# Optimization experiments

Measured on AMD Instinct MI355X. Metric: run time of the kernel, lower is better.

## Reference

```python
import jax, jax.numpy as jnp
import numpy as np

ARRAY_NUM = 1024
LENS_NUM = 16384
LENS_W = 128      # sqrt(LENS_NUM)
SUB = LENS_W // 2  # 64
N_ANG = 121       # fixed by get_weights(): arange(-60, 61)
SLG = 0.1         # side_lobe_gain
VAR_GAIN = 200.0  # 2D lens


def setup_inputs() -> dict:
    key = jax.random.key(0)
    ks = jax.random.split(key, 8)
    u = lambda k, s: jax.random.uniform(k, s, dtype=jnp.float32)
    n = lambda k, s: jax.random.normal(k, s, dtype=jnp.float32)
    return {
        "w_re": u(ks[0], (61, ARRAY_NUM)),
        "w_im": u(ks[1], (61, ARRAY_NUM)),
        "theta_re": u(ks[2], (SUB * SUB, 1)),
        "theta_im": u(ks[3], (SUB * SUB, 1)),
        "G_re": n(ks[4], (ARRAY_NUM, LENS_NUM)),
        "G_im": n(ks[5], (ARRAY_NUM, LENS_NUM)),
        "sv_re": n(ks[6], (LENS_NUM, N_ANG)),
        "sv_im": n(ks[7], (LENS_NUM, N_ANG)),
    }


def _side_lobe_loss(w_re, w_im, theta_re, theta_im, G_re, G_im, sv_re, sv_im):
    w = w_re + 1j * w_im  # [61, A] complex64
    # get_w: clamp |w| to >= 1, normalize, mirror (flipud+fliplr) to full 121 rows
    wn = w / jnp.maximum(jnp.abs(w), 1.0)
    w_full = jnp.concatenate([wn, wn[::-1, ::-1][1:]], axis=0)  # [121, A]

    # get_theta (2D): normalize, tile 4-fold symmetric [128,128], flatten
    theta = theta_re + 1j * theta_im  # [SUB*SUB, 1]
    theta = theta / jnp.abs(theta)
    ts = theta.reshape(SUB, SUB)
    row = jnp.concatenate([ts, ts[:, ::-1]], axis=1)      # [SUB, 2*SUB]
    full = jnp.concatenate([row, row[::-1, :]], axis=0)   # [2*SUB, 2*SUB]
    theta_vec = full.reshape(-1)                          # [LENS_NUM]

    G = G_re + 1j * G_im        # [A, L]
    sv = sv_re + 1j * sv_im     # [L, N_ANG]

    lens_in = w_full @ G                     # [121, L]
    # matmul with diag(theta) == elementwise scale along L (same math)
    sout_c = (lens_in * theta_vec[None, :]) @ sv  # [121, 121]
    sout = (jnp.abs(sout_c) ** 2) / ARRAY_NUM / LENS_NUM

    x = jnp.arange(-60, 61, dtype=jnp.float32)
    weights = (-0.2 / 3600.0) * x ** 2 + 1.0  # [121]

    d = jnp.diagonal(sout)
    diag_out = jnp.sum(d)
    var_loss = VAR_GAIN * jnp.std(d / weights, ddof=1)  # torch.std is unbiased

    # sidelobe cancel: sum of diagonals ti in [-5, 5]
    idx = jnp.arange(N_ANG)
    band = (jnp.abs(idx[:, None] - idx[None, :]) <= 5).astype(sout.dtype)
    diag_sum = jnp.sum(sout * band)
    amp_loss = -diag_out + SLG * (jnp.sum(sout) - diag_sum)

    reg = 0.0 * jnp.mean(jnp.abs(w) ** 2)  # zero-weight reg term, kept for fidelity
    return amp_loss + var_loss + reg


def reference(w_re, w_im, theta_re, theta_im, G_re, G_im, sv_re, sv_im):
    return _side_lobe_loss(w_re, w_im, theta_re, theta_im, G_re, G_im, sv_re, sv_im)
```

## Files before the change

kernel.cpp:

```cpp
#include <hip/hip_runtime.h>
#include <math.h>

#define A_NUM 1024
#define L_NUM 16384
#define NANG  121
#define NPAD  256
#define KSPLIT 32
#define TA 64
#define CHUNK_L 32
#define CHUNK_K 64
#define ROWP 72
#define NCHUNK_G 512

#define WS_TV   0u
#define WS_WF   131072u
#define WS_BT   1122304u
#define WS_PART 19996672u
#define WS_C    53551104u
#define WS_SOUT 54599680u

typedef float  f32x4  __attribute__((ext_vector_type(4)));
typedef short  s16x8  __attribute__((ext_vector_type(8)));
typedef unsigned short u16x8 __attribute__((ext_vector_type(8)));
typedef unsigned short u16x4 __attribute__((ext_vector_type(4)));

__device__ __forceinline__ unsigned short f2bf(float x) {
    union { float f; unsigned u; } v; v.f = x;
    unsigned r = v.u + 0x7fffu + ((v.u >> 16) & 1u);
    return (unsigned short)(r >> 16);
}

#define GLOAD_LDS16(SRC, DST) \
    __builtin_amdgcn_global_load_lds((const __attribute__((address_space(1))) void*)(SRC), \
                                     (__attribute__((address_space(3))) void*)(DST), 16, 0, 0)

__global__ __launch_bounds__(256) void k_prep(
    const float* __restrict__ w_re, const float* __restrict__ w_im,
    const float* __restrict__ th_re, const float* __restrict__ th_im,
    char* __restrict__ wsb)
{
    int idx = blockIdx.x * 256 + threadIdx.x;
    float* tv = (float*)(wsb + WS_TV);
    float* wf = (float*)(wsb + WS_WF);
    if (idx < 16384) {
        int i = idx >> 7, j = idx & 127;
        int r = (i < 64) ? i : 127 - i;
        int c = (j < 64) ? j : 127 - j;
        float tr = th_re[r * 64 + c], ti = th_im[r * 64 + c];
        float inv = rsqrtf(tr * tr + ti * ti);
        tv[2 * idx]     = tr * inv;
        tv[2 * idx + 1] = ti * inv;
    } else if (idx < 16384 + 121 * 1024) {
        int e = idx - 16384;
        int r = e >> 10, a = e & 1023;
        int sr = (r < 61) ? r : 120 - r;
        int sa = (r < 61) ? a : 1023 - a;
        float wr = w_re[sr * 1024 + sa], wi = w_im[sr * 1024 + sa];
        float mag = sqrtf(wr * wr + wi * wi);
        float s = (mag > 1.0f) ? (1.0f / mag) : 1.0f;
        wf[2 * e]     = wr * s;
        wf[2 * e + 1] = wi * s;
    }
}

__global__ __launch_bounds__(256) void k_prep_bt(
    const float* __restrict__ sv_re, const float* __restrict__ sv_im,
    char* __restrict__ wsb)
{
    __shared__ float lsr[32][121];
    __shared__ float lsi[32][121];
    const int cg = blockIdx.x;
    const int t  = threadIdx.x;
    const int lbase = cg * 32;
    for (int e = t; e < 32 * 121; e += 256) {
        int l = e / 121, n = e - l * 121;
        lsr[l][n] = sv_re[(size_t)(lbase + l) * 121 + n];
        lsi[l][n] = sv_im[(size_t)(lbase + l) * 121 + n];
    }
    __syncthreads();
    unsigned short* bt = (unsigned short*)(wsb + WS_BT) + (size_t)cg * (NPAD * ROWP);
    #pragma unroll
    for (int i = 0; i < 18; ++i) {
        int o = t + i * 256;
        int n = o / 18;
        int j = o - n * 18;
        int kl0 = j * 4;
        u16x4 val;
        #pragma unroll
        for (int q = 0; q < 4; ++q) {
            int kl = kl0 + q;
            float v = 0.0f;
            if (kl < 64) {
                int lloc = kl >> 1;
                if (n < 121)                     v = (kl & 1) ? -lsi[lloc][n] : lsr[lloc][n];
                else if (n >= 128 && n < 249)    { int m = n - 128; v = (kl & 1) ? lsr[lloc][m] : lsi[lloc][m]; }
            }
            val[q] = f2bf(v);
        }
        *(u16x4*)&bt[(size_t)o * 4] = val;
    }
}

__global__ __launch_bounds__(256, 2) void k_gemm1(
    const float* __restrict__ G_re, const float* __restrict__ G_im,
    char* __restrict__ wsb)
{
    __shared__ __align__(16) unsigned short lA[TA * ROWP];
    __shared__ __align__(16) unsigned short lB[NPAD * ROWP];

    const int t = threadIdx.x;
    const int bid = blockIdx.x;
    const int kidx  = bid & 31;
    const int atile = bid >> 5;
    const int a0 = atile * TA;
    const int l_begin = kidx * 512;

    const float* __restrict__ tvF = (const float*)(wsb + WS_TV);
    const unsigned short* __restrict__ BtG = (const unsigned short*)(wsb + WS_BT);

    const int wid = t >> 6, lane = t & 63;
    const int arow = lane & 15;
    const int koff = (lane >> 4) * 8;

    const int arow_s = t >> 3;
    const int slot   = t & 7;
    const int lloc   = slot * 4;

    f32x4 acc[4][4];
    #pragma unroll
    for (int j = 0; j < 4; ++j)
        #pragma unroll
        for (int s = 0; s < 4; ++s) acc[j][s] = (f32x4)(0.0f);

    for (int c = 0; c < 16; ++c) {
        const int l0 = l_begin + c * CHUNK_L;
        #pragma unroll
        for (int p = 0; p < 2; ++p) {
            const int a = p * 32 + arow_s;
            const float* grp = G_re + (size_t)(a0 + a) * L_NUM + l0 + lloc;
            const float* gip = G_im + (size_t)(a0 + a) * L_NUM + l0 + lloc;
            float4 gr = *(const float4*)grp;
            float4 gi = *(const float4*)gip;
            const float* tvp = tvF + 2 * (l0 + lloc);
            float4 t0 = *(const float4*)tvp;
            float4 t1 = *(const float4*)(tvp + 4);
            u16x8 pk;
            pk[0] = f2bf(gr.x * t0.x - gi.x * t0.y); pk[1] = f2bf(gr.x * t0.y + gi.x * t0.x);
            pk[2] = f2bf(gr.y * t0.z - gi.y * t0.w); pk[3] = f2bf(gr.y * t0.w + gi.y * t0.z);
            pk[4] = f2bf(gr.z * t1.x - gi.z * t1.y); pk[5] = f2bf(gr.z * t1.y + gi.z * t1.x);
            pk[6] = f2bf(gr.w * t1.z - gi.w * t1.w); pk[7] = f2bf(gr.w * t1.w + gi.w * t1.z);
            *(u16x8*)&lA[a * ROWP + slot * 8] = pk;
        }
        {
            const int cgk = kidx * 16 + c;
            const unsigned short* bsrc = BtG + (size_t)cgk * (NPAD * ROWP);
            unsigned short* ldsb = lB + (size_t)(t & ~63) * 8;
            const unsigned short* gsrc = bsrc + (size_t)t * 8;
            #pragma unroll
            for (int i = 0; i < 9; ++i) {
                GLOAD_LDS16(gsrc + (size_t)i * 2048, ldsb + (size_t)i * 2048);
            }
        }
        __syncthreads();
        #pragma unroll
        for (int kh = 0; kh < 2; ++kh) {
            s16x8 af[4], bf[4];
            #pragma unroll
            for (int j = 0; j < 4; ++j)
                af[j] = *(const s16x8*)&lA[(j * 16 + arow) * ROWP + kh * 32 + koff];
            #pragma unroll
            for (int s = 0; s < 4; ++s)
                bf[s] = *(const s16x8*)&lB[(wid * 64 + s * 16 + arow) * ROWP + kh * 32 + koff];
            #pragma unroll
            for (int j = 0; j < 4; ++j)
                #pragma unroll
                for (int s = 0; s < 4; ++s)
                    acc[j][s] = __builtin_amdgcn_mfma_f32_16x16x32_bf16(af[j], bf[s], acc[j][s], 0, 0, 0);
        }
        __syncthreads();
    }

    float* part = (float*)(wsb + WS_PART) + (size_t)kidx * (A_NUM * NPAD);
    #pragma unroll
    for (int j = 0; j < 4; ++j) {
        #pragma unroll
        for (int s = 0; s < 4; ++s) {
            const int col  = wid * 64 + s * 16 + (lane & 15);
            const int rowb = a0 + j * 16 + (lane >> 4) * 4;
            f32x4 v = acc[j][s];
            #pragma unroll
            for (int r = 0; r < 4; ++r)
                part[(size_t)(rowb + r) * NPAD + col] = v[r];
        }
    }
}

__global__ __launch_bounds__(256) void k_reduce_part(char* __restrict__ wsb)
{
    const int e = blockIdx.x * 256 + threadIdx.x;
    const float* part = (const float*)(wsb + WS_PART);
    float s = 0.0f;
    #pragma unroll
    for (int p = 0; p < KSPLIT; ++p) s += part[(size_t)p * (A_NUM * NPAD) + e];
    ((float*)(wsb + WS_C))[e] = s;
}

__global__ __launch_bounds__(128) void k_gemm2(char* __restrict__ wsb)
{
    __shared__ float lw[2048];
    const int r = blockIdx.x;
    const int t = threadIdx.x;
    const float* wf = (const float*)(wsb + WS_WF) + r * 2048;
    #pragma unroll
    for (int k = 0; k < 16; ++k) lw[t + k * 128] = wf[t + k * 128];
    __syncthreads();
    if (t < 121) {
        const float* __restrict__ C = (const float*)(wsb + WS_C);
        float re = 0.0f, im = 0.0f;
        for (int a = 0; a < 1024; a += 8) {
            #pragma unroll
            for (int u = 0; u < 8; ++u) {
                float wr = lw[2 * (a + u)], wi = lw[2 * (a + u) + 1];
                float br = C[(size_t)(a + u) * NPAD + t];
                float bi = C[(size_t)(a + u) * NPAD + 128 + t];
                re += wr * br - wi * bi;
                im += wr * bi + wi * br;
            }
        }
        ((float*)(wsb + WS_SOUT))[r * 121 + t] = (re * re + im * im) * (1.0f / 16777216.0f);
    }
}

__global__ __launch_bounds__(256) void k_final(const char* __restrict__ wsb, float* __restrict__ out)
{
    __shared__ float red[256];
    __shared__ float red2[256];
    __shared__ float dsh[121];
    const int t = threadIdx.x;
    const float* __restrict__ sout = (const float*)(wsb + WS_SOUT);
    float tot = 0.0f, band = 0.0f;
    for (int e = t; e < NANG * NANG; e += 256) {
        float v = sout[e];
        int i = e / NANG;
        int j = e - i * NANG;
        tot += v;
        int dd = i - j; if (dd < 0) dd = -dd;
        if (dd <= 5) band += v;
        if (dd == 0) dsh[i] = v;
    }
    red[t] = tot; red2[t] = band;
    __syncthreads();
    for (int s2 = 128; s2 > 0; s2 >>= 1) {
        if (t < s2) { red[t] += red[t + s2]; red2[t] += red2[t + s2]; }
        __syncthreads();
    }
    float total = red[0], bandsum = red2[0];
    __syncthreads();

    float d = 0.0f, y = 0.0f;
    if (t < NANG) {
        d = dsh[t];
        float x = (float)(t - 60);
        float wgt = fmaf(x * x, -0.2f / 3600.0f, 1.0f);
        y = d / wgt;
    }
    red[t] = d; red2[t] = y;
    __syncthreads();
    for (int s2 = 128; s2 > 0; s2 >>= 1) {
        if (t < s2) { red[t] += red[t + s2]; red2[t] += red2[t + s2]; }
        __syncthreads();
    }
    float diag_sum = red[0];
    float mean = red2[0] * (1.0f / 121.0f);
    __syncthreads();

    float dev = (t < NANG) ? (y - mean) : 0.0f;
    red[t] = dev * dev;
    __syncthreads();
    for (int s2 = 128; s2 > 0; s2 >>= 1) {
        if (t < s2) { red[t] += red[t + s2]; }
        __syncthreads();
    }
    if (t == 0) {
        float var = red[0] * (1.0f / 120.0f);
        float std_ = sqrtf(var);
        float amp = -diag_sum + 0.1f * (total - bandsum);
        out[0] = amp + 200.0f * std_;
    }
}

extern "C" void kernel_launch(void* const* d_in, const int* in_sizes, int n_in,
                              void* d_out, int out_size, void* d_ws, size_t ws_size,
                              hipStream_t stream)
{
    const float* w_re  = (const float*)d_in[0];
    const float* w_im  = (const float*)d_in[1];
    const float* th_re = (const float*)d_in[2];
    const float* th_im = (const float*)d_in[3];
    const float* G_re  = (const float*)d_in[4];
    const float* G_im  = (const float*)d_in[5];
    const float* sv_re = (const float*)d_in[6];
    const float* sv_im = (const float*)d_in[7];
    char* wsb  = (char*)d_ws;
    float* out = (float*)d_out;

    k_prep<<<dim3(548), 256, 0, stream>>>(w_re, w_im, th_re, th_im, wsb);
    k_prep_bt<<<dim3(NCHUNK_G), 256, 0, stream>>>(sv_re, sv_im, wsb);
    k_gemm1<<<dim3(512), 256, 0, stream>>>(G_re, G_im, wsb);
    k_reduce_part<<<dim3(1024), 256, 0, stream>>>(wsb);
    k_gemm2<<<dim3(121), 128, 0, stream>>>(wsb);
    k_final<<<dim3(1), 256, 0, stream>>>(wsb, out);
}
```

Measured before the change: 265.4 us.

## Double-buffer GEMM1 with larger A tile and parallelize reduce and GEMM2

The main GEMM kernel now uses 512-thread blocks covering 128 A rows and double-buffers both the A and B tiles in LDS. Global loads for the next chunk are issued before the MFMAs on the current chunk, and theta is staged once in LDS. The split-K reduction is vectorized to float4, and GEMM2 splits the 1024-term sum across four thread groups combined through LDS. k_prep_bt is also reworked to write rows directly. The intended gain is less load latency exposure and fewer kernel-level inefficiencies, at the cost of more LDS use and only 256 blocks for GEMM1, which lowers grid-level parallelism.

```diff
diff --git a/kernel.cpp b/kernel.cpp
--- a/kernel.cpp
+++ b/kernel.cpp
@@ -6,11 +6,9 @@
 #define NANG  121
 #define NPAD  256
 #define KSPLIT 32
-#define TA 64
-#define CHUNK_L 32
-#define CHUNK_K 64
+#define TA 128
+#define NCH 16
 #define ROWP 72
-#define NCHUNK_G 512
 
 #define WS_TV   0u
 #define WS_WF   131072u
@@ -19,10 +17,10 @@
 #define WS_C    53551104u
 #define WS_SOUT 54599680u
 
+typedef unsigned short ushort_t;
 typedef float  f32x4  __attribute__((ext_vector_type(4)));
 typedef short  s16x8  __attribute__((ext_vector_type(8)));
 typedef unsigned short u16x8 __attribute__((ext_vector_type(8)));
-typedef unsigned short u16x4 __attribute__((ext_vector_type(4)));
 
 __device__ __forceinline__ unsigned short f2bf(float x) {
     union { float f; unsigned u; } v; v.f = x;
@@ -67,64 +65,127 @@
     const float* __restrict__ sv_re, const float* __restrict__ sv_im,
     char* __restrict__ wsb)
 {
-    __shared__ float lsr[32][121];
-    __shared__ float lsi[32][121];
+    __shared__ float lsr[32][128];
+    __shared__ float lsi[32][128];
     const int cg = blockIdx.x;
     const int t  = threadIdx.x;
     const int lbase = cg * 32;
-    for (int e = t; e < 32 * 121; e += 256) {
-        int l = e / 121, n = e - l * 121;
-        lsr[l][n] = sv_re[(size_t)(lbase + l) * 121 + n];
-        lsi[l][n] = sv_im[(size_t)(lbase + l) * 121 + n];
-    }
-    __syncthreads();
-    unsigned short* bt = (unsigned short*)(wsb + WS_BT) + (size_t)cg * (NPAD * ROWP);
-    #pragma unroll
-    for (int i = 0; i < 18; ++i) {
-        int o = t + i * 256;
-        int n = o / 18;
-        int j = o - n * 18;
-        int kl0 = j * 4;
-        u16x4 val;
-        #pragma unroll
-        for (int q = 0; q < 4; ++q) {
-            int kl = kl0 + q;
-            float v = 0.0f;
-            if (kl < 64) {
-                int lloc = kl >> 1;
-                if (n < 121)                     v = (kl & 1) ? -lsi[lloc][n] : lsr[lloc][n];
-                else if (n >= 128 && n < 249)    { int m = n - 128; v = (kl & 1) ? lsr[lloc][m] : lsi[lloc][m]; }
+    for (int e = t; e < 4096; e += 256) {
+        int l = e >> 7, n = e & 127;
+        float vr = 0.0f, vi = 0.0f;
+        if (n < 121) {
+            vr = sv_re[(size_t)(lbase + l) * 121 + n];
+            vi = sv_im[(size_t)(lbase + l) * 121 + n];
+        }
+        lsr[l][n] = vr; lsi[l][n] = vi;
+    }
+    __syncthreads();
+    ushort_t* bt = (ushort_t*)(wsb + WS_BT) + (size_t)cg * (NPAD * ROWP);
+    const int m = t - 128;
+    #pragma unroll
+    for (int kk = 0; kk < 9; ++kk) {
+        u16x8 v;
+        #pragma unroll
+        for (int qq = 0; qq < 8; ++qq) {
+            int k = kk * 8 + qq;
+            float x = 0.0f;
+            if (k < 64) {
+                int l = k >> 1;
+                if (t < 121)                       x = (k & 1) ? -lsi[l][t] : lsr[l][t];
+                else if (t >= 128 && t < 249)      x = (k & 1) ?  lsr[l][m] : lsi[l][m];
             }
-            val[q] = f2bf(v);
-        }
-        *(u16x4*)&bt[(size_t)o * 4] = val;
-    }
-}
-
-__global__ __launch_bounds__(256, 2) void k_gemm1(
+            v[qq] = f2bf(x);
+        }
+        *(u16x8*)&bt[(size_t)t * ROWP + kk * 8] = v;
+    }
+}
+
+struct APf { float4 gr0, gr1, gi0, gi1; };
+
+__device__ __forceinline__ APf a_issue(const float* __restrict__ G_re, const float* __restrict__ G_im,
+                                       size_t rowbase, int loff) {
+    APf p;
+    const float* grp = G_re + rowbase + loff;
+    const float* gip = G_im + rowbase + loff;
+    p.gr0 = *(const float4*)grp;       p.gr1 = *(const float4*)(grp + 4);
+    p.gi0 = *(const float4*)gip;       p.gi1 = *(const float4*)(gip + 4);
+    return p;
+}
+
+__device__ __forceinline__ void a_store(const APf& p, const float* __restrict__ ltv,
+                                        ushort_t* __restrict__ lAb, int c, int arow, int aslot) {
+    const float* tp = ltv + c * 64 + aslot * 16;
+    float4 t0 = *(const float4*)tp;
+    float4 t1 = *(const float4*)(tp + 4);
+    float4 t2 = *(const float4*)(tp + 8);
+    float4 t3 = *(const float4*)(tp + 12);
+    u16x8 k0, k1;
+    k0[0] = f2bf(p.gr0.x * t0.x - p.gi0.x * t0.y);  k0[1] = f2bf(p.gr0.x * t0.y + p.gi0.x * t0.x);
+    k0[2] = f2bf(p.gr0.y * t0.z - p.gi0.y * t0.w);  k0[3] = f2bf(p.gr0.y * t0.w + p.gi0.y * t0.z);
+    k0[4] = f2bf(p.gr0.z * t1.x - p.gi0.z * t1.y);  k0[5] = f2bf(p.gr0.z * t1.y + p.gi0.z * t1.x);
+    k0[6] = f2bf(p.gr0.w * t1.z - p.gi0.w * t1.w);  k0[7] = f2bf(p.gr0.w * t1.w + p.gi0.w * t1.z);
+    k1[0] = f2bf(p.gr1.x * t2.x - p.gi1.x * t2.y);  k1[1] = f2bf(p.gr1.x * t2.y + p.gi1.x * t2.x);
+    k1[2] = f2bf(p.gr1.y * t2.z - p.gi1.y * t2.w);  k1[3] = f2bf(p.gr1.y * t2.w + p.gi1.y * t2.z);
+    k1[4] = f2bf(p.gr1.z * t3.x - p.gi1.z * t3.y);  k1[5] = f2bf(p.gr1.z * t3.y + p.gi1.z * t3.x);
+    k1[6] = f2bf(p.gr1.w * t3.z - p.gi1.w * t3.w);  k1[7] = f2bf(p.gr1.w * t3.w + p.gi1.w * t3.z);
+    *(u16x8*)&lAb[arow * ROWP + aslot * 16]     = k0;
+    *(u16x8*)&lAb[arow * ROWP + aslot * 16 + 8] = k1;
+}
+
+__device__ __forceinline__ void b_issue(const ushort_t* __restrict__ bsrc,
+                                        ushort_t* __restrict__ lBb, int w, int lane) {
+    #pragma unroll
+    for (int i = 0; i < 5; ++i) {
+        int seg = w + 8 * i;
+        if (seg < 36)
+            GLOAD_LDS16(bsrc + seg * 512 + lane * 8, lBb + seg * 512);
+    }
+}
+
+__device__ __forceinline__ void do_mfma(const ushort_t* __restrict__ lAb, const ushort_t* __restrict__ lBb,
+                                        f32x4 (&acc)[4][4], int wa, int wn, int lane) {
+    const int fr = lane & 15;
+    const int fk = (lane >> 4) * 8;
+    #pragma unroll
+    for (int kh = 0; kh < 2; ++kh) {
+        s16x8 af[4], bf[4];
+        #pragma unroll
+        for (int j = 0; j < 4; ++j)
+            af[j] = *(const s16x8*)&lAb[(wa * 64 + j * 16 + fr) * ROWP + kh * 32 + fk];
+        #pragma unroll
+        for (int s = 0; s < 4; ++s)
+            bf[s] = *(const s16x8*)&lBb[(wn * 64 + s * 16 + fr) * ROWP + kh * 32 + fk];
+        #pragma unroll
+        for (int j = 0; j < 4; ++j)
+            #pragma unroll
+            for (int s = 0; s < 4; ++s)
+                acc[j][s] = __builtin_amdgcn_mfma_f32_16x16x32_bf16(af[j], bf[s], acc[j][s], 0, 0, 0);
+    }
+}
+
+__global__ __launch_bounds__(512, 2) void k_gemm1(
     const float* __restrict__ G_re, const float* __restrict__ G_im,
     char* __restrict__ wsb)
 {
-    __shared__ __align__(16) unsigned short lA[TA * ROWP];
-    __shared__ __align__(16) unsigned short lB[NPAD * ROWP];
+    __shared__ __align__(16) ushort_t lA[2][TA * ROWP];
+    __shared__ __align__(16) ushort_t lB[2][NPAD * ROWP];
+    __shared__ __align__(16) float ltv[1024];
 
     const int t = threadIdx.x;
-    const int bid = blockIdx.x;
-    const int kidx  = bid & 31;
-    const int atile = bid >> 5;
+    const int lane = t & 63, w = t >> 6;
+    const int kidx  = blockIdx.x & 31;
+    const int atile = blockIdx.x >> 5;
     const int a0 = atile * TA;
     const int l_begin = kidx * 512;
 
     const float* __restrict__ tvF = (const float*)(wsb + WS_TV);
-    const unsigned short* __restrict__ BtG = (const unsigned short*)(wsb + WS_BT);
-
-    const int wid = t >> 6, lane = t & 63;
-    const int arow = lane & 15;
-    const int koff = (lane >> 4) * 8;
-
-    const int arow_s = t >> 3;
-    const int slot   = t & 7;
-    const int lloc   = slot * 4;
+    const ushort_t* __restrict__ BtG = (const ushort_t*)(wsb + WS_BT);
+
+    *(float2*)&ltv[2 * t] = *(const float2*)&tvF[2 * l_begin + 2 * t];
+
+    const int arow = t >> 2, aslot = t & 3;
+    const size_t rowbase = (size_t)(a0 + arow) * L_NUM + l_begin;
+    const int wa = w & 1, wn = w >> 1;
 
     f32x4 acc[4][4];
     #pragma unroll
@@ -132,61 +193,33 @@
         #pragma unroll
         for (int s = 0; s < 4; ++s) acc[j][s] = (f32x4)(0.0f);
 
-    for (int c = 0; c < 16; ++c) {
-        const int l0 = l_begin + c * CHUNK_L;
-        #pragma unroll
-        for (int p = 0; p < 2; ++p) {
-            const int a = p * 32 + arow_s;
-            const float* grp = G_re + (size_t)(a0 + a) * L_NUM + l0 + lloc;
-            const float* gip = G_im + (size_t)(a0 + a) * L_NUM + l0 + lloc;
-            float4 gr = *(const float4*)grp;
-            float4 gi = *(const float4*)gip;
-            const float* tvp = tvF + 2 * (l0 + lloc);
-            float4 t0 = *(const float4*)tvp;
-            float4 t1 = *(const float4*)(tvp + 4);
-            u16x8 pk;
-            pk[0] = f2bf(gr.x * t0.x - gi.x * t0.y); pk[1] = f2bf(gr.x * t0.y + gi.x * t0.x);
-            pk[2] = f2bf(gr.y * t0.z - gi.y * t0.w); pk[3] = f2bf(gr.y * t0.w + gi.y * t0.z);
-            pk[4] = f2bf(gr.z * t1.x - gi.z * t1.y); pk[5] = f2bf(gr.z * t1.y + gi.z * t1.x);
-            pk[6] = f2bf(gr.w * t1.z - gi.w * t1.w); pk[7] = f2bf(gr.w * t1.w + gi.w * t1.z);
-            *(u16x8*)&lA[a * ROWP + slot * 8] = pk;
-        }
-        {
-            const int cgk = kidx * 16 + c;
-            const unsigned short* bsrc = BtG + (size_t)cgk * (NPAD * ROWP);
-            unsigned short* ldsb = lB + (size_t)(t & ~63) * 8;
-            const unsigned short* gsrc = bsrc + (size_t)t * 8;
-            #pragma unroll
-            for (int i = 0; i < 9; ++i) {
-                GLOAD_LDS16(gsrc + (size_t)i * 2048, ldsb + (size_t)i * 2048);
-            }
-        }
-        __syncthreads();
-        #pragma unroll
-        for (int kh = 0; kh < 2; ++kh) {
-            s16x8 af[4], bf[4];
-            #pragma unroll
-            for (int j = 0; j < 4; ++j)
-                af[j] = *(const s16x8*)&lA[(j * 16 + arow) * ROWP + kh * 32 + koff];
-            #pragma unroll
-            for (int s = 0; s < 4; ++s)
-                bf[s] = *(const s16x8*)&lB[(wid * 64 + s * 16 + arow) * ROWP + kh * 32 + koff];
-            #pragma unroll
-            for (int j = 0; j < 4; ++j)
-                #pragma unroll
-                for (int s = 0; s < 4; ++s)
-                    acc[j][s] = __builtin_amdgcn_mfma_f32_16x16x32_bf16(af[j], bf[s], acc[j][s], 0, 0, 0);
-        }
-        __syncthreads();
+    APf p0 = a_issue(G_re, G_im, rowbase, aslot * 8);
+    b_issue(BtG + (size_t)(kidx * 16) * (NPAD * ROWP), lB[0], w, lane);
+    __syncthreads();
+    a_store(p0, ltv, lA[0], 0, arow, aslot);
+    __syncthreads();
+
+    for (int c = 0; c < NCH; ++c) {
+        const int cur = c & 1;
+        if (c + 1 < NCH) {
+            APf pn = a_issue(G_re, G_im, rowbase, (c + 1) * 32 + aslot * 8);
+            b_issue(BtG + (size_t)(kidx * 16 + c + 1) * (NPAD * ROWP), lB[cur ^ 1], w, lane);
+            do_mfma(lA[cur], lB[cur], acc, wa, wn, lane);
+            a_store(pn, ltv, lA[cur ^ 1], c + 1, arow, aslot);
+            __syncthreads();
+        } else {
+            do_mfma(lA[cur], lB[cur], acc, wa, wn, lane);
+        }
     }
 
     float* part = (float*)(wsb + WS_PART) + (size_t)kidx * (A_NUM * NPAD);
+    const int fr = lane & 15, fq = lane >> 4;
     #pragma unroll
     for (int j = 0; j < 4; ++j) {
         #pragma unroll
         for (int s = 0; s < 4; ++s) {
-            const int col  = wid * 64 + s * 16 + (lane & 15);
-            const int rowb = a0 + j * 16 + (lane >> 4) * 4;
+            const int col  = wn * 64 + s * 16 + fr;
+            const int rowb = a0 + wa * 64 + j * 16 + fq * 4;
             f32x4 v = acc[j][s];
             #pragma unroll
             for (int r = 0; r < 4; ++r)
@@ -197,37 +230,45 @@
 
 __global__ __launch_bounds__(256) void k_reduce_part(char* __restrict__ wsb)
 {
-    const int e = blockIdx.x * 256 + threadIdx.x;
-    const float* part = (const float*)(wsb + WS_PART);
-    float s = 0.0f;
-    #pragma unroll
-    for (int p = 0; p < KSPLIT; ++p) s += part[(size_t)p * (A_NUM * NPAD) + e];
-    ((float*)(wsb + WS_C))[e] = s;
-}
-
-__global__ __launch_bounds__(128) void k_gemm2(char* __restrict__ wsb)
+    const int e4 = blockIdx.x * 256 + threadIdx.x;
+    const f32x4* part = (const f32x4*)(wsb + WS_PART);
+    f32x4 s = part[e4];
+    #pragma unroll
+    for (int p = 1; p < KSPLIT; ++p) s += part[(size_t)p * 65536 + e4];
+    ((f32x4*)(wsb + WS_C))[e4] = s;
+}
+
+__global__ __launch_bounds__(512) void k_gemm2(char* __restrict__ wsb)
 {
     __shared__ float lw[2048];
+    __shared__ float rre[4][128];
+    __shared__ float rim[4][128];
     const int r = blockIdx.x;
     const int t = threadIdx.x;
     const float* wf = (const float*)(wsb + WS_WF) + r * 2048;
-    #pragma unroll
-    for (int k = 0; k < 16; ++k) lw[t + k * 128] = wf[t + k * 128];
+    *(float4*)&lw[4 * t] = *(const float4*)&wf[4 * t];
+    __syncthreads();
+    const int q = t >> 7, n = t & 127;
+    const float* __restrict__ C = (const float*)(wsb + WS_C);
+    const float* __restrict__ Cb = C + (size_t)q * 256 * 256 + n;
+    const float* __restrict__ lwb = lw + q * 512;
+    float re = 0.0f, im = 0.0f;
+    for (int a8 = 0; a8 < 256; a8 += 8) {
+        #pragma unroll
+        for (int u = 0; u < 8; ++u) {
+            float wr = lwb[2 * (a8 + u)], wi = lwb[2 * (a8 + u) + 1];
+            float br = Cb[(size_t)(a8 + u) * 256];
+            float bi = Cb[(size_t)(a8 + u) * 256 + 128];
+            re += wr * br - wi * bi;
+            im += wr * bi + wi * br;
+        }
+    }
+    rre[q][n] = re; rim[q][n] = im;
     __syncthreads();
     if (t < 121) {
-        const float* __restrict__ C = (const float*)(wsb + WS_C);
-        float re = 0.0f, im = 0.0f;
-        for (int a = 0; a < 1024; a += 8) {
-            #pragma unroll
-            for (int u = 0; u < 8; ++u) {
-                float wr = lw[2 * (a + u)], wi = lw[2 * (a + u) + 1];
-                float br = C[(size_t)(a + u) * NPAD + t];
-                float bi = C[(size_t)(a + u) * NPAD + 128 + t];
-                re += wr * br - wi * bi;
-                im += wr * bi + wi * br;
-            }
-        }
-        ((float*)(wsb + WS_SOUT))[r * 121 + t] = (re * re + im * im) * (1.0f / 16777216.0f);
+        float rr = rre[0][t] + rre[1][t] + rre[2][t] + rre[3][t];
+        float ii = rim[0][t] + rim[1][t] + rim[2][t] + rim[3][t];
+        ((float*)(wsb + WS_SOUT))[r * 121 + t] = (rr * rr + ii * ii) * (1.0f / 16777216.0f);
     }
 }
 
@@ -305,9 +346,9 @@
     float* out = (float*)d_out;
 
     k_prep<<<dim3(548), 256, 0, stream>>>(w_re, w_im, th_re, th_im, wsb);
-    k_prep_bt<<<dim3(NCHUNK_G), 256, 0, stream>>>(sv_re, sv_im, wsb);
-    k_gemm1<<<dim3(512), 256, 0, stream>>>(G_re, G_im, wsb);
-    k_reduce_part<<<dim3(1024), 256, 0, stream>>>(wsb);
-    k_gemm2<<<dim3(121), 128, 0, stream>>>(wsb);
+    k_prep_bt<<<dim3(512), 256, 0, stream>>>(sv_re, sv_im, wsb);
+    k_gemm1<<<dim3(256), 512, 0, stream>>>(G_re, G_im, wsb);
+    k_reduce_part<<<dim3(256), 256, 0, stream>>>(wsb);
+    k_gemm2<<<dim3(121), 512, 0, stream>>>(wsb);
     k_final<<<dim3(1), 256, 0, stream>>>(wsb, out);
 }
```

Measured after the change: 240.6 us. 1.1x faster.
